# Performance work log

Measured on AMD Instinct MI355X. Metric: run time of the kernel, lower is better.

The kernel has to match this reference:

```python
import jax, jax.numpy as jnp
import numpy as np

H = 8
D_MODEL = 512
D_K = D_MODEL // H


def setup_inputs() -> dict:
    key = jax.random.key(0)
    ks = jax.random.split(key, 12)
    B, S = 4, 2048
    scale = 1.0 / np.sqrt(D_MODEL)
    inp = {
        "query": jax.random.normal(ks[0], (B, S, D_MODEL), jnp.float32),
        "key": jax.random.normal(ks[1], (B, S, D_MODEL), jnp.float32),
        "value": jax.random.normal(ks[2], (B, S, D_MODEL), jnp.float32),
        "mask": jnp.ones((B, 1, S), jnp.int32),
        "Wq": jax.random.normal(ks[3], (D_MODEL, D_MODEL), jnp.float32) * scale,
        "bq": jax.random.normal(ks[4], (D_MODEL,), jnp.float32) * 0.01,
        "Wk": jax.random.normal(ks[5], (D_MODEL, D_MODEL), jnp.float32) * scale,
        "bk": jax.random.normal(ks[6], (D_MODEL,), jnp.float32) * 0.01,
        "Wv": jax.random.normal(ks[7], (D_MODEL, D_MODEL), jnp.float32) * scale,
        "bv": jax.random.normal(ks[8], (D_MODEL,), jnp.float32) * 0.01,
        "Wo": jax.random.normal(ks[9], (D_MODEL, D_MODEL), jnp.float32) * scale,
        "bo": jax.random.normal(ks[10], (D_MODEL,), jnp.float32) * 0.01,
    }
    return inp


def reference(query, key, value, mask, Wq, bq, Wk, bk, Wv, bv, Wo, bo):
    B, S, _ = query.shape

    def proj(x, W, b):
        # [B,S,D] -> [B,H,S,d_k]
        y = jnp.einsum('bsd,ed->bse', x, W) + b  # torch Linear: x @ W.T + b
        return y.reshape(B, S, H, D_K).transpose(0, 2, 1, 3)

    q = proj(query, Wq, bq)
    k = proj(key, Wk, bk)
    v = proj(value, Wv, bv)

    scores = jnp.einsum('bhqd,bhkd->bhqk', q, k) / jnp.sqrt(jnp.float32(D_K))
    m = mask[:, None, :, :]  # [B,1,1,S]
    scores = jnp.where(m == 0, jnp.float32(-1e9), scores)
    p_attn = jax.nn.softmax(scores, axis=-1)  # dropout is identity in eval
    x = jnp.einsum('bhqk,bhkd->bhqd', p_attn, v)
    x = x.transpose(0, 2, 1, 3).reshape(B, S, D_MODEL)
    return jnp.einsum('bsd,ed->bse', x, Wo) + bo
```

## Files before the change

### kernel.cpp

```cpp
#include <hip/hip_runtime.h>
#include <hip/hip_bf16.h>

#define H 8
#define DMODEL 512
#define DK 64
#define BATCH 4
#define SEQ 2048
#define M_TOTAL (BATCH*SEQ)

typedef short bf16x8 __attribute__((ext_vector_type(8)));
typedef float f32x4 __attribute__((ext_vector_type(4)));

__device__ __forceinline__ unsigned short f2bf(float f) {
    unsigned int u = __builtin_bit_cast(unsigned int, f);
    u += 0x7FFFu + ((u >> 16) & 1u);
    return (unsigned short)(u >> 16);
}

__device__ __forceinline__ unsigned int pack_bf2(float a, float b) {
    unsigned int r;
    asm("v_cvt_pk_bf16_f32 %0, %1, %2" : "=v"(r) : "v"(a), "v"(b));
    return r;
}

__device__ __forceinline__ float exp2_fast(float x) {
    float r;
    asm("v_exp_f32 %0, %1" : "=v"(r) : "v"(x));
    return r;
}

__global__ __launch_bounds__(256) void gemm_qkv(
    const float* __restrict__ query, const float* __restrict__ key_,
    const float* __restrict__ value,
    const float* __restrict__ Wq, const float* __restrict__ bq,
    const float* __restrict__ Wk, const float* __restrict__ bk,
    const float* __restrict__ Wv, const float* __restrict__ bv,
    unsigned short* __restrict__ Qh, unsigned short* __restrict__ Kh,
    unsigned short* __restrict__ Vt)
{
    const int z = blockIdx.z;
    const float* A    = (z == 0) ? query : (z == 1) ? key_ : value;
    const float* W    = (z == 0) ? Wq : (z == 1) ? Wk : Wv;
    const float* bias = (z == 0) ? bq : (z == 1) ? bk : bv;
    unsigned short* out = (z == 0) ? Qh : (z == 1) ? Kh : Vt;

    const int m0 = blockIdx.x * 128;
    const int n0 = blockIdx.y * 64;
    const int tid = threadIdx.x;
    const int lane = tid & 63;
    const int w = tid >> 6;
    const int g = lane >> 4, qi = lane & 15;
    const int wm = w >> 1, wn = w & 1;

    __shared__ unsigned short Alds[128 * 40];
    __shared__ unsigned short Blds[64 * 40];

    f32x4 acc[4][2];
    #pragma unroll
    for (int i = 0; i < 4; i++)
        #pragma unroll
        for (int j = 0; j < 2; j++) acc[i][j] = f32x4{0.f, 0.f, 0.f, 0.f};

    float4 aA[4], bA[2], aB[4], bB[2];

    auto ld = [&](float4 (&ar)[4], float4 (&br)[2], int k0) {
        #pragma unroll
        for (int i = 0; i < 4; i++) { int idx = tid + i * 256;
            ar[i] = *(const float4*)(A + (size_t)(m0 + (idx >> 3)) * 512 + k0 + (idx & 7) * 4); }
        #pragma unroll
        for (int i = 0; i < 2; i++) { int idx = tid + i * 256;
            br[i] = *(const float4*)(W + (size_t)(n0 + (idx >> 3)) * 512 + k0 + (idx & 7) * 4); }
    };
    auto st = [&](float4 (&ar)[4], float4 (&br)[2]) {
        #pragma unroll
        for (int i = 0; i < 4; i++) { int idx = tid + i * 256;
            uint2 p; p.x = pack_bf2(ar[i].x, ar[i].y); p.y = pack_bf2(ar[i].z, ar[i].w);
            *(uint2*)(Alds + (idx >> 3) * 40 + (idx & 7) * 4) = p; }
        #pragma unroll
        for (int i = 0; i < 2; i++) { int idx = tid + i * 256;
            uint2 p; p.x = pack_bf2(br[i].x, br[i].y); p.y = pack_bf2(br[i].z, br[i].w);
            *(uint2*)(Blds + (idx >> 3) * 40 + (idx & 7) * 4) = p; }
    };
    auto tile = [&]() {
        bf16x8 af[4], bf[2];
        #pragma unroll
        for (int mt = 0; mt < 4; mt++)
            af[mt] = *(const bf16x8*)(Alds + (wm * 64 + mt * 16 + qi) * 40 + g * 8);
        #pragma unroll
        for (int nt = 0; nt < 2; nt++)
            bf[nt] = *(const bf16x8*)(Blds + (wn * 32 + nt * 16 + qi) * 40 + g * 8);
        #pragma unroll
        for (int mt = 0; mt < 4; mt++)
            #pragma unroll
            for (int nt = 0; nt < 2; nt++)
                acc[mt][nt] = __builtin_amdgcn_mfma_f32_16x16x32_bf16(af[mt], bf[nt], acc[mt][nt], 0, 0, 0);
    };

    ld(aA, bA, 0);
    for (int k0 = 0; k0 < 512; k0 += 64) {
        __syncthreads();
        st(aA, bA);
        ld(aB, bB, k0 + 32);
        __syncthreads();
        tile();
        __syncthreads();
        st(aB, bB);
        if (k0 + 64 < 512) ld(aA, bA, k0 + 64);
        __syncthreads();
        tile();
    }

    #pragma unroll
    for (int mt = 0; mt < 4; mt++) {
        int mbase = m0 + wm * 64 + mt * 16 + g * 4;
        #pragma unroll
        for (int nt = 0; nt < 2; nt++) {
            int n = n0 + wn * 32 + nt * 16 + qi;
            float bv = bias[n];
            int h = n >> 6, dk = n & 63;
            if (z == 2) {
                int b = mbase >> 11, s = mbase & 2047;
                uint2 pk;
                pk.x = pack_bf2(acc[mt][nt][0] + bv, acc[mt][nt][1] + bv);
                pk.y = pack_bf2(acc[mt][nt][2] + bv, acc[mt][nt][3] + bv);
                *(uint2*)(out + ((size_t)(b * H + h) * 64 + dk) * SEQ + s) = pk;
            } else {
                float sc = (z == 0) ? 0.18033688011112042f : 1.0f;
                #pragma unroll
                for (int r = 0; r < 4; r++) {
                    int m = mbase + r;
                    int b = m >> 11, s = m & 2047;
                    out[((size_t)(b * H + h) * SEQ + s) * 64 + dk] = f2bf((acc[mt][nt][r] + bv) * sc);
                }
            }
        }
    }
}

__global__ __launch_bounds__(256) void gemm_o(
    const unsigned short* __restrict__ Xa, const float* __restrict__ W,
    const float* __restrict__ bias, float* __restrict__ out)
{
    const int m0 = blockIdx.x * 128;
    const int n0 = blockIdx.y * 64;
    const int tid = threadIdx.x;
    const int lane = tid & 63;
    const int w = tid >> 6;
    const int g = lane >> 4, qi = lane & 15;
    const int wm = w >> 1, wn = w & 1;

    __shared__ unsigned short Alds[128 * 40];
    __shared__ unsigned short Blds[64 * 40];

    f32x4 acc[4][2];
    #pragma unroll
    for (int i = 0; i < 4; i++)
        #pragma unroll
        for (int j = 0; j < 2; j++) acc[i][j] = f32x4{0.f, 0.f, 0.f, 0.f};

    bf16x8 aA[2], aB[2];
    float4 bA[2], bB[2];

    auto ld = [&](bf16x8 (&ar)[2], float4 (&br)[2], int k0) {
        #pragma unroll
        for (int i = 0; i < 2; i++) { int idx = tid + i * 256;
            ar[i] = *(const bf16x8*)(Xa + (size_t)(m0 + (idx >> 2)) * 512 + k0 + (idx & 3) * 8); }
        #pragma unroll
        for (int i = 0; i < 2; i++) { int idx = tid + i * 256;
            br[i] = *(const float4*)(W + (size_t)(n0 + (idx >> 3)) * 512 + k0 + (idx & 7) * 4); }
    };
    auto st = [&](bf16x8 (&ar)[2], float4 (&br)[2]) {
        #pragma unroll
        for (int i = 0; i < 2; i++) { int idx = tid + i * 256;
            *(bf16x8*)(Alds + (idx >> 2) * 40 + (idx & 3) * 8) = ar[i]; }
        #pragma unroll
        for (int i = 0; i < 2; i++) { int idx = tid + i * 256;
            uint2 p; p.x = pack_bf2(br[i].x, br[i].y); p.y = pack_bf2(br[i].z, br[i].w);
            *(uint2*)(Blds + (idx >> 3) * 40 + (idx & 7) * 4) = p; }
    };
    auto tile = [&]() {
        bf16x8 af[4], bf[2];
        #pragma unroll
        for (int mt = 0; mt < 4; mt++)
            af[mt] = *(const bf16x8*)(Alds + (wm * 64 + mt * 16 + qi) * 40 + g * 8);
        #pragma unroll
        for (int nt = 0; nt < 2; nt++)
            bf[nt] = *(const bf16x8*)(Blds + (wn * 32 + nt * 16 + qi) * 40 + g * 8);
        #pragma unroll
        for (int mt = 0; mt < 4; mt++)
            #pragma unroll
            for (int nt = 0; nt < 2; nt++)
                acc[mt][nt] = __builtin_amdgcn_mfma_f32_16x16x32_bf16(af[mt], bf[nt], acc[mt][nt], 0, 0, 0);
    };

    ld(aA, bA, 0);
    for (int k0 = 0; k0 < 512; k0 += 64) {
        __syncthreads();
        st(aA, bA);
        ld(aB, bB, k0 + 32);
        __syncthreads();
        tile();
        __syncthreads();
        st(aB, bB);
        if (k0 + 64 < 512) ld(aA, bA, k0 + 64);
        __syncthreads();
        tile();
    }

    #pragma unroll
    for (int mt = 0; mt < 4; mt++) {
        int mbase = m0 + wm * 64 + mt * 16 + g * 4;
        #pragma unroll
        for (int nt = 0; nt < 2; nt++) {
            int n = n0 + wn * 32 + nt * 16 + qi;
            float bv = bias[n];
            #pragma unroll
            for (int r = 0; r < 4; r++)
                out[(size_t)(mbase + r) * 512 + n] = acc[mt][nt][r] + bv;
        }
    }
}

__global__ __launch_bounds__(256) void attn_kernel(
    const unsigned short* __restrict__ Qh,
    const unsigned short* __restrict__ Kh,
    const unsigned short* __restrict__ Vt,
    const int* __restrict__ mask,
    unsigned short* __restrict__ Xattn)
{
    const int tid = threadIdx.x;
    const int lane = tid & 63;
    const int w = tid >> 6;
    const int g = lane >> 4;
    const int qi = lane & 15;
    const int s3 = qi & 7;

    const int bid = blockIdx.x;
    const int xcd = bid & 7;
    const int slot = bid >> 3;
    const int bh = xcd * 4 + (slot >> 4);
    const int q0 = (slot & 15) * 128;
    const int b = bh >> 3;

    __shared__ unsigned short Klds[3][64 * 64];
    __shared__ unsigned short Vlds[3][64 * 64];
    __shared__ unsigned short Plds[4][32 * 64];
    __shared__ int amflag;

    bf16x8 qf[2][2];
    #pragma unroll
    for (int f = 0; f < 2; f++) {
        const unsigned short* Qbase =
            Qh + ((size_t)bh * SEQ + q0 + w * 32 + f * 16 + qi) * 64 + g * 8;
        qf[f][0] = *(const bf16x8*)(Qbase);
        qf[f][1] = *(const bf16x8*)(Qbase + 32);
    }

    f32x4 acc_o[2][4];
    #pragma unroll
    for (int f = 0; f < 2; f++)
        #pragma unroll
        for (int dt = 0; dt < 4; dt++) acc_o[f][dt] = f32x4{0.f, 0.f, 0.f, 0.f};
    float l_lane[2] = {0.f, 0.f};

    const unsigned char* Kbh = (const unsigned char*)(Kh + (size_t)bh * SEQ * 64);
    const unsigned char* Vbh = (const unsigned char*)(Vt + (size_t)bh * 64 * SEQ);
    const int* maskb = mask + b * SEQ;

    if (tid == 0) amflag = 1;
    __syncthreads();
    {
        int v = 1;
        #pragma unroll
        for (int i = 0; i < 8; i++) v &= (maskb[tid + i * 256] != 0) ? 1 : 0;
        if (__ballot(v != 0) != ~0ull && lane == 0) amflag = 0;
    }
    __syncthreads();
    const bool allmask = (amflag != 0);

    const int klane = ((lane >> 3) << 7)  + (((lane & 7) ^ (lane >> 3)) << 4);
    const int vlane = ((lane >> 3) << 12) + (((lane & 7) ^ (lane >> 3)) << 4);

    const int rb0 = qi * 128 + ((g ^ s3) << 4);
    const unsigned char* PldsB = (const unsigned char*)&Plds[w][0];
    const int pw0 = qi * 128 + (((g >> 1) ^ s3) << 4) + ((g & 1) << 3);

    auto stage = [&](const unsigned char* ks, const unsigned char* vs, int buf) {
        unsigned char* kd = (unsigned char*)&Klds[buf][0];
        unsigned char* vd = (unsigned char*)&Vlds[buf][0];
        #pragma unroll
        for (int j = 0; j < 2; j++) {
            const int c = w + 4 * j;
            __builtin_amdgcn_global_load_lds(
                (const __attribute__((address_space(1))) unsigned int*)(ks + c * 1024),
                (__attribute__((address_space(3))) unsigned int*)(kd + c * 1024), 16, 0, 0);
            __builtin_amdgcn_global_load_lds(
                (const __attribute__((address_space(1))) unsigned int*)(vs + c * 32768),
                (__attribute__((address_space(3))) unsigned int*)(vd + c * 1024), 16, 0, 0);
        }
    };

    auto compute = [&](int t, int buf) {
        const int kv0 = t << 6;
        const unsigned char* KB = (const unsigned char*)&Klds[buf][0];
        const unsigned char* VB = (const unsigned char*)&Vlds[buf][0];

        f32x4 sacc[2][4];
        __builtin_amdgcn_s_setprio(1);
        #pragma unroll
        for (int nt = 0; nt < 4; nt++) {
            bf16x8 kf0 = *(const bf16x8*)(KB + (rb0 ^ 0)  + nt * 2048);
            bf16x8 kf1 = *(const bf16x8*)(KB + (rb0 ^ 64) + nt * 2048);
            #pragma unroll
            for (int f = 0; f < 2; f++) {
                f32x4 sa = f32x4{0.f, 0.f, 0.f, 0.f};
                sa = __builtin_amdgcn_mfma_f32_16x16x32_bf16(kf0, qf[f][0], sa, 0, 0, 0);
                sa = __builtin_amdgcn_mfma_f32_16x16x32_bf16(kf1, qf[f][1], sa, 0, 0, 0);
                sacc[f][nt] = sa;
            }
        }
        __builtin_amdgcn_s_setprio(0);

        if (!allmask) {
            const unsigned long long mb = __ballot(maskb[kv0 + lane] != 0);
            if (mb != ~0ull) {
                #pragma unroll
                for (int f = 0; f < 2; f++)
                    #pragma unroll
                    for (int nt = 0; nt < 4; nt++)
                        #pragma unroll
                        for (int r = 0; r < 4; r++) {
                            int kvl = nt * 16 + g * 4 + r;
                            if (!((mb >> kvl) & 1ull)) sacc[f][nt][r] = -1e9f;
                        }
            }
        }

        #pragma unroll
        for (int f = 0; f < 2; f++) {
            #pragma unroll
            for (int nt = 0; nt < 4; nt++) {
                float p0 = exp2_fast(sacc[f][nt][0]);
                float p1 = exp2_fast(sacc[f][nt][1]);
                float p2 = exp2_fast(sacc[f][nt][2]);
                float p3 = exp2_fast(sacc[f][nt][3]);
                l_lane[f] += (p0 + p1) + (p2 + p3);
                uint2 pk;
                pk.x = pack_bf2(p0, p1);
                pk.y = pack_bf2(p2, p3);
                *(uint2*)((unsigned char*)&Plds[w][0] + f * 2048 +
                          (pw0 ^ (nt << 5))) = pk;
            }
        }

        __builtin_amdgcn_s_setprio(1);
        #pragma unroll
        for (int kt = 0; kt < 2; kt++) {
            bf16x8 pf0 = *(const bf16x8*)(PldsB + 0    + (rb0 ^ (kt << 6)));
            bf16x8 pf1 = *(const bf16x8*)(PldsB + 2048 + (rb0 ^ (kt << 6)));
            #pragma unroll
            for (int dt = 0; dt < 4; dt++) {
                bf16x8 vf = *(const bf16x8*)(VB + (rb0 ^ (kt << 6)) + dt * 2048);
                acc_o[0][dt] = __builtin_amdgcn_mfma_f32_16x16x32_bf16(vf, pf0, acc_o[0][dt], 0, 0, 0);
                acc_o[1][dt] = __builtin_amdgcn_mfma_f32_16x16x32_bf16(vf, pf1, acc_o[1][dt], 0, 0, 0);
            }
        }
        __builtin_amdgcn_s_setprio(0);
    };

    const unsigned char* ks = Kbh + klane;
    const unsigned char* vs = Vbh + vlane;

    stage(ks, vs, 0); ks += 8192; vs += 128;
    stage(ks, vs, 1); ks += 8192; vs += 128;
    int bc = 0, bs = 2;
    #pragma unroll 1
    for (int t = 0; t < 32; ++t) {
        if (t < 31) __builtin_amdgcn_s_waitcnt(0xF74);
        else        __builtin_amdgcn_s_waitcnt(0xF70);
        __builtin_amdgcn_s_barrier();
        compute(t, bc);
        if (t + 2 < 32) {
            stage(ks, vs, bs);
            ks += 8192; vs += 128;
        }
        bc = (bc == 2) ? 0 : bc + 1;
        bs = (bs == 2) ? 0 : bs + 1;
    }

    const int h = bh & 7;
    #pragma unroll
    for (int f = 0; f < 2; f++) {
        float l = l_lane[f];
        l += __shfl_xor(l, 16);
        l += __shfl_xor(l, 32);
        const float inv = 1.0f / l;
        const int s = q0 + w * 32 + f * 16 + qi;
        size_t base = ((size_t)b * SEQ + s) * 512 + h * 64;
        #pragma unroll
        for (int dt = 0; dt < 4; dt++) {
            uint2 o;
            o.x = pack_bf2(acc_o[f][dt][0] * inv, acc_o[f][dt][1] * inv);
            o.y = pack_bf2(acc_o[f][dt][2] * inv, acc_o[f][dt][3] * inv);
            *(uint2*)(Xattn + base + dt * 16 + g * 4) = o;
        }
    }
}

extern "C" void kernel_launch(void* const* d_in, const int* in_sizes, int n_in,
                              void* d_out, int out_size, void* d_ws, size_t ws_size,
                              hipStream_t stream)
{
    const float* query = (const float*)d_in[0];
    const float* key_  = (const float*)d_in[1];
    const float* value = (const float*)d_in[2];
    const int*   mask  = (const int*)d_in[3];
    const float* Wq = (const float*)d_in[4];
    const float* bq = (const float*)d_in[5];
    const float* Wk = (const float*)d_in[6];
    const float* bk = (const float*)d_in[7];
    const float* Wv = (const float*)d_in[8];
    const float* bv = (const float*)d_in[9];
    const float* Wo = (const float*)d_in[10];
    const float* bo = (const float*)d_in[11];

    unsigned short* Qh = (unsigned short*)d_ws;
    unsigned short* Kh = Qh + (size_t)M_TOTAL * DMODEL;
    unsigned short* Vt = Kh + (size_t)M_TOTAL * DMODEL;
    unsigned short* Xa = Vt + (size_t)M_TOTAL * DMODEL;

    dim3 thr(256);
    hipLaunchKernelGGL(gemm_qkv, dim3(64, 8, 3), thr, 0, stream,
                       query, key_, value, Wq, bq, Wk, bk, Wv, bv, Qh, Kh, Vt);
    hipLaunchKernelGGL(attn_kernel, dim3(512), thr, 0, stream, Qh, Kh, Vt, mask, Xa);
    hipLaunchKernelGGL(gemm_o, dim3(64, 8), thr, 0, stream, Xa, Wo, bo, (float*)d_out);
}
```

Baseline: 94.78 us.

## Split attention block into 8 waves of 16 query rows each

The attention kernel goes from 4 waves handling 32 query rows each to 8 waves handling 16 rows each, at the same 128 queries per block. Each wave now issues one K and one V async load per stage instead of two, and the waitcnt is adjusted to match. The goal is more waves per CU to hide LDS and exp latency, with fewer registers per wave. In exchange, each K/V fragment read from LDS is reused across only one Q tile, which doubles LDS read traffic per MFMA.

Result: faster. 90.27 us (-4.8%).

```diff
diff --git a/kernel.cpp b/kernel.cpp
--- a/kernel.cpp
+++ b/kernel.cpp
@@ -221,7 +221,7 @@
     }
 }
 
-__global__ __launch_bounds__(256) void attn_kernel(
+__global__ __launch_bounds__(512, 4) void attn_kernel(
     const unsigned short* __restrict__ Qh,
     const unsigned short* __restrict__ Kh,
     const unsigned short* __restrict__ Vt,
@@ -244,24 +244,21 @@
 
     __shared__ unsigned short Klds[3][64 * 64];
     __shared__ unsigned short Vlds[3][64 * 64];
-    __shared__ unsigned short Plds[4][32 * 64];
+    __shared__ unsigned short Plds[8][16 * 64];
     __shared__ int amflag;
 
-    bf16x8 qf[2][2];
-    #pragma unroll
-    for (int f = 0; f < 2; f++) {
+    bf16x8 qf0, qf1;
+    {
         const unsigned short* Qbase =
-            Qh + ((size_t)bh * SEQ + q0 + w * 32 + f * 16 + qi) * 64 + g * 8;
-        qf[f][0] = *(const bf16x8*)(Qbase);
-        qf[f][1] = *(const bf16x8*)(Qbase + 32);
-    }
-
-    f32x4 acc_o[2][4];
-    #pragma unroll
-    for (int f = 0; f < 2; f++)
-        #pragma unroll
-        for (int dt = 0; dt < 4; dt++) acc_o[f][dt] = f32x4{0.f, 0.f, 0.f, 0.f};
-    float l_lane[2] = {0.f, 0.f};
+            Qh + ((size_t)bh * SEQ + q0 + w * 16 + qi) * 64 + g * 8;
+        qf0 = *(const bf16x8*)(Qbase);
+        qf1 = *(const bf16x8*)(Qbase + 32);
+    }
+
+    f32x4 acc_o[4];
+    #pragma unroll
+    for (int dt = 0; dt < 4; dt++) acc_o[dt] = f32x4{0.f, 0.f, 0.f, 0.f};
+    float l_lane = 0.f;
 
     const unsigned char* Kbh = (const unsigned char*)(Kh + (size_t)bh * SEQ * 64);
     const unsigned char* Vbh = (const unsigned char*)(Vt + (size_t)bh * 64 * SEQ);
@@ -272,7 +269,7 @@
     {
         int v = 1;
         #pragma unroll
-        for (int i = 0; i < 8; i++) v &= (maskb[tid + i * 256] != 0) ? 1 : 0;
+        for (int i = 0; i < 4; i++) v &= (maskb[tid + i * 512] != 0) ? 1 : 0;
         if (__ballot(v != 0) != ~0ull && lane == 0) amflag = 0;
     }
     __syncthreads();
@@ -282,22 +279,19 @@
     const int vlane = ((lane >> 3) << 12) + (((lane & 7) ^ (lane >> 3)) << 4);
 
     const int rb0 = qi * 128 + ((g ^ s3) << 4);
-    const unsigned char* PldsB = (const unsigned char*)&Plds[w][0];
+    unsigned char* Pw = (unsigned char*)&Plds[w][0];
     const int pw0 = qi * 128 + (((g >> 1) ^ s3) << 4) + ((g & 1) << 3);
 
     auto stage = [&](const unsigned char* ks, const unsigned char* vs, int buf) {
         unsigned char* kd = (unsigned char*)&Klds[buf][0];
         unsigned char* vd = (unsigned char*)&Vlds[buf][0];
-        #pragma unroll
-        for (int j = 0; j < 2; j++) {
-            const int c = w + 4 * j;
-            __builtin_amdgcn_global_load_lds(
-                (const __attribute__((address_space(1))) unsigned int*)(ks + c * 1024),
-                (__attribute__((address_space(3))) unsigned int*)(kd + c * 1024), 16, 0, 0);
-            __builtin_amdgcn_global_load_lds(
-                (const __attribute__((address_space(1))) unsigned int*)(vs + c * 32768),
-                (__attribute__((address_space(3))) unsigned int*)(vd + c * 1024), 16, 0, 0);
-        }
+        const int c = w;
+        __builtin_amdgcn_global_load_lds(
+            (const __attribute__((address_space(1))) unsigned int*)(ks + c * 1024),
+            (__attribute__((address_space(3))) unsigned int*)(kd + c * 1024), 16, 0, 0);
+        __builtin_amdgcn_global_load_lds(
+            (const __attribute__((address_space(1))) unsigned int*)(vs + c * 32768),
+            (__attribute__((address_space(3))) unsigned int*)(vd + c * 1024), 16, 0, 0);
     };
 
     auto compute = [&](int t, int buf) {
@@ -305,19 +299,16 @@
         const unsigned char* KB = (const unsigned char*)&Klds[buf][0];
         const unsigned char* VB = (const unsigned char*)&Vlds[buf][0];
 
-        f32x4 sacc[2][4];
+        f32x4 sacc[4];
         __builtin_amdgcn_s_setprio(1);
         #pragma unroll
         for (int nt = 0; nt < 4; nt++) {
             bf16x8 kf0 = *(const bf16x8*)(KB + (rb0 ^ 0)  + nt * 2048);
             bf16x8 kf1 = *(const bf16x8*)(KB + (rb0 ^ 64) + nt * 2048);
-            #pragma unroll
-            for (int f = 0; f < 2; f++) {
-                f32x4 sa = f32x4{0.f, 0.f, 0.f, 0.f};
-                sa = __builtin_amdgcn_mfma_f32_16x16x32_bf16(kf0, qf[f][0], sa, 0, 0, 0);
-                sa = __builtin_amdgcn_mfma_f32_16x16x32_bf16(kf1, qf[f][1], sa, 0, 0, 0);
-                sacc[f][nt] = sa;
-            }
+            f32x4 sa = f32x4{0.f, 0.f, 0.f, 0.f};
+            sa = __builtin_amdgcn_mfma_f32_16x16x32_bf16(kf0, qf0, sa, 0, 0, 0);
+            sa = __builtin_amdgcn_mfma_f32_16x16x32_bf16(kf1, qf1, sa, 0, 0, 0);
+            sacc[nt] = sa;
         }
         __builtin_amdgcn_s_setprio(0);
 
@@ -325,44 +316,36 @@
             const unsigned long long mb = __ballot(maskb[kv0 + lane] != 0);
             if (mb != ~0ull) {
                 #pragma unroll
-                for (int f = 0; f < 2; f++)
+                for (int nt = 0; nt < 4; nt++)
                     #pragma unroll
-                    for (int nt = 0; nt < 4; nt++)
-                        #pragma unroll
-                        for (int r = 0; r < 4; r++) {
-                            int kvl = nt * 16 + g * 4 + r;
-                            if (!((mb >> kvl) & 1ull)) sacc[f][nt][r] = -1e9f;
-                        }
+                    for (int r = 0; r < 4; r++) {
+                        int kvl = nt * 16 + g * 4 + r;
+                        if (!((mb >> kvl) & 1ull)) sacc[nt][r] = -1e9f;
+                    }
             }
         }
 
         #pragma unroll
-        for (int f = 0; f < 2; f++) {
-            #pragma unroll
-            for (int nt = 0; nt < 4; nt++) {
-                float p0 = exp2_fast(sacc[f][nt][0]);
-                float p1 = exp2_fast(sacc[f][nt][1]);
-                float p2 = exp2_fast(sacc[f][nt][2]);
-                float p3 = exp2_fast(sacc[f][nt][3]);
-                l_lane[f] += (p0 + p1) + (p2 + p3);
-                uint2 pk;
-                pk.x = pack_bf2(p0, p1);
-                pk.y = pack_bf2(p2, p3);
-                *(uint2*)((unsigned char*)&Plds[w][0] + f * 2048 +
-                          (pw0 ^ (nt << 5))) = pk;
-            }
+        for (int nt = 0; nt < 4; nt++) {
+            float p0 = exp2_fast(sacc[nt][0]);
+            float p1 = exp2_fast(sacc[nt][1]);
+            float p2 = exp2_fast(sacc[nt][2]);
+            float p3 = exp2_fast(sacc[nt][3]);
+            l_lane += (p0 + p1) + (p2 + p3);
+            uint2 pk;
+            pk.x = pack_bf2(p0, p1);
+            pk.y = pack_bf2(p2, p3);
+            *(uint2*)(Pw + (pw0 ^ (nt << 5))) = pk;
         }
 
         __builtin_amdgcn_s_setprio(1);
         #pragma unroll
         for (int kt = 0; kt < 2; kt++) {
-            bf16x8 pf0 = *(const bf16x8*)(PldsB + 0    + (rb0 ^ (kt << 6)));
-            bf16x8 pf1 = *(const bf16x8*)(PldsB + 2048 + (rb0 ^ (kt << 6)));
+            bf16x8 pf = *(const bf16x8*)(Pw + (rb0 ^ (kt << 6)));
             #pragma unroll
             for (int dt = 0; dt < 4; dt++) {
                 bf16x8 vf = *(const bf16x8*)(VB + (rb0 ^ (kt << 6)) + dt * 2048);
-                acc_o[0][dt] = __builtin_amdgcn_mfma_f32_16x16x32_bf16(vf, pf0, acc_o[0][dt], 0, 0, 0);
-                acc_o[1][dt] = __builtin_amdgcn_mfma_f32_16x16x32_bf16(vf, pf1, acc_o[1][dt], 0, 0, 0);
+                acc_o[dt] = __builtin_amdgcn_mfma_f32_16x16x32_bf16(vf, pf, acc_o[dt], 0, 0, 0);
             }
         }
         __builtin_amdgcn_s_setprio(0);
@@ -376,7 +359,7 @@
     int bc = 0, bs = 2;
     #pragma unroll 1
     for (int t = 0; t < 32; ++t) {
-        if (t < 31) __builtin_amdgcn_s_waitcnt(0xF74);
+        if (t < 31) __builtin_amdgcn_s_waitcnt(0xF72);
         else        __builtin_amdgcn_s_waitcnt(0xF70);
         __builtin_amdgcn_s_barrier();
         compute(t, bc);
@@ -389,21 +372,18 @@
     }
 
     const int h = bh & 7;
-    #pragma unroll
-    for (int f = 0; f < 2; f++) {
-        float l = l_lane[f];
-        l += __shfl_xor(l, 16);
-        l += __shfl_xor(l, 32);
-        const float inv = 1.0f / l;
-        const int s = q0 + w * 32 + f * 16 + qi;
-        size_t base = ((size_t)b * SEQ + s) * 512 + h * 64;
-        #pragma unroll
-        for (int dt = 0; dt < 4; dt++) {
-            uint2 o;
-            o.x = pack_bf2(acc_o[f][dt][0] * inv, acc_o[f][dt][1] * inv);
-            o.y = pack_bf2(acc_o[f][dt][2] * inv, acc_o[f][dt][3] * inv);
-            *(uint2*)(Xattn + base + dt * 16 + g * 4) = o;
-        }
+    float l = l_lane;
+    l += __shfl_xor(l, 16);
+    l += __shfl_xor(l, 32);
+    const float inv = 1.0f / l;
+    const int s = q0 + w * 16 + qi;
+    size_t base = ((size_t)b * SEQ + s) * 512 + h * 64;
+    #pragma unroll
+    for (int dt = 0; dt < 4; dt++) {
+        uint2 o;
+        o.x = pack_bf2(acc_o[dt][0] * inv, acc_o[dt][1] * inv);
+        o.y = pack_bf2(acc_o[dt][2] * inv, acc_o[dt][3] * inv);
+        *(uint2*)(Xattn + base + dt * 16 + g * 4) = o;
     }
 }
 
@@ -429,9 +409,8 @@
     unsigned short* Vt = Kh + (size_t)M_TOTAL * DMODEL;
     unsigned short* Xa = Vt + (size_t)M_TOTAL * DMODEL;
 
-    dim3 thr(256);
-    hipLaunchKernelGGL(gemm_qkv, dim3(64, 8, 3), thr, 0, stream,
+    hipLaunchKernelGGL(gemm_qkv, dim3(64, 8, 3), dim3(256), 0, stream,
                        query, key_, value, Wq, bq, Wk, bk, Wv, bv, Qh, Kh, Vt);
-    hipLaunchKernelGGL(attn_kernel, dim3(512), thr, 0, stream, Qh, Kh, Vt, mask, Xa);
-    hipLaunchKernelGGL(gemm_o, dim3(64, 8), thr, 0, stream, Xa, Wo, bo, (float*)d_out);
-}
+    hipLaunchKernelGGL(attn_kernel, dim3(512), dim3(512), 0, stream, Qh, Kh, Vt, mask, Xa);
+    hipLaunchKernelGGL(gemm_o, dim3(64, 8), dim3(256), 0, stream, Xa, Wo, bo, (float*)d_out);
+}
```
